# Performance work log

Measured on AMD Instinct MI355X. Metric: run time of the kernel, lower is better.

Reference implementation:

```python
import jax, jax.numpy as jnp
import numpy as np

ALPHA = 0.25
GAMMA = 2.0
DELTA = 0.5
BREAK_W = 1.0
REG_W = 1.0
CLASS_WEIGHT_TABLE = jnp.array([1.0, 4.0, 3.0, 2.0], dtype=jnp.float32)  # classes 0..3
LOG_CLAMP = -100.0  # torch BCELoss clamps log terms at -100

B, T = 2048, 16384


def setup_inputs() -> dict:
    key = jax.random.key(0)
    k1, k2, k3, k4 = jax.random.split(key, 4)
    break_predictions = jax.random.uniform(k1, (B, T), dtype=jnp.float32)
    regression_predictions = jax.random.uniform(k2, (B, T), dtype=jnp.float32) * 3.0
    break_targets = jax.random.uniform(k3, (B, T), dtype=jnp.float32)
    regression_targets = jax.random.uniform(k4, (B, T), dtype=jnp.float32) * 3.0
    return {
        "break_predictions": break_predictions,
        "regression_predictions": regression_predictions,
        "break_targets": break_targets,
        "regression_targets": regression_targets,
    }


def _bce(p, t):
    # torch BCELoss: mean of -(t*log(p) + (1-t)*log(1-p)), logs clamped at -100
    log_p = jnp.maximum(jnp.log(p), LOG_CLAMP)
    log_1p = jnp.maximum(jnp.log1p(-p), LOG_CLAMP)
    return jnp.mean(-(t * log_p + (1.0 - t) * log_1p))


def _duration_aware_focal(y_pred, y_true):
    y_pred = y_pred.reshape(-1)
    y_true = y_true.reshape(-1)
    # class-weight gather: round + clamp to [0,3], index a 4-entry table
    cls_idx = jnp.clip(jnp.round(y_true), 0.0, 3.0).astype(jnp.int32)
    weights = CLASS_WEIGHT_TABLE[cls_idx]
    d = jnp.abs(y_pred - y_true)
    focal = jnp.clip(d / DELTA, 0.0, 1.0) ** GAMMA
    # smooth L1 with beta=DELTA
    base = jnp.where(d < DELTA, 0.5 * d * d / DELTA, d - 0.5 * DELTA)
    return jnp.mean(ALPHA * focal * base * weights)


def reference(break_predictions, regression_predictions, break_targets, regression_targets):
    bt = jnp.clip(break_targets, 0.0, 1.0)
    bp = jnp.clip(break_predictions, 0.0, 1.0)
    break_loss = _bce(bp, bt)
    regression_loss = _duration_aware_focal(regression_predictions, regression_targets)
    total = BREAK_W * break_loss + REG_W * regression_loss
    return (total, break_loss, regression_loss)
```

## Files before the change

### kernel.cpp

```cpp
#include <hip/hip_runtime.h>


constexpr int BLOCK = 256;
constexpr int HGRID = 2048;
constexpr int GRID  = 2 * HGRID;

__device__ __forceinline__ void bce_elem(float pv, float tv, float& acc) {
    constexpr float CLAMP2 = -144.26950408889634f;
    float pc = fminf(fmaxf(pv, 0.0f), 1.0f);
    float tc = fminf(fmaxf(tv, 0.0f), 1.0f);
    float lp  = fmaxf(__log2f(pc),        CLAMP2);
    float l1p = fmaxf(__log2f(1.0f - pc), CLAMP2);
    acc -= l1p + tc * (lp - l1p);
}

__device__ __forceinline__ void focal_elem(float qv, float sv, float& acc) {
    float d = fabsf(qv - sv);
    float f = fminf(d + d, 1.0f);
    float base = (d < 0.5f) ? (d * d) : (d - 0.25f);
    float r = fminf(fmaxf(__builtin_rintf(sv), 0.0f), 3.0f);
    float w = (r == 0.0f) ? 1.0f : (r == 1.0f) ? 4.0f : (r == 2.0f) ? 3.0f : 2.0f;
    acc += (f * f) * base * w;
}

__global__ __launch_bounds__(BLOCK) void partial_kernel(
    const float4* __restrict__ bp4, const float4* __restrict__ rp4,
    const float4* __restrict__ bt4, const float4* __restrict__ rt4,
    float* __restrict__ partials, int n4, int n)
{
    const int stride = HGRID * BLOCK;
    float a0 = 0.0f, a1 = 0.0f;
    const bool isB = (blockIdx.x < HGRID);
    const int  vb  = isB ? blockIdx.x : blockIdx.x - HGRID;

    if (isB) {
        for (int i = vb * BLOCK + threadIdx.x; i < n4; i += stride) {
            float4 p = bp4[i];
            float4 t = bt4[i];
            bce_elem(p.x, t.x, a0);
            bce_elem(p.y, t.y, a1);
            bce_elem(p.z, t.z, a0);
            bce_elem(p.w, t.w, a1);
        }
        if (vb == 0) {
            const float* bp = (const float*)bp4;
            const float* bt = (const float*)bt4;
            for (int k = n4 * 4 + threadIdx.x; k < n; k += BLOCK)
                bce_elem(bp[k], bt[k], a0);
        }
    } else {
        for (int i = vb * BLOCK + threadIdx.x; i < n4; i += stride) {
            float4 q = rp4[i];
            float4 s = rt4[i];
            focal_elem(q.x, s.x, a0);
            focal_elem(q.y, s.y, a1);
            focal_elem(q.z, s.z, a0);
            focal_elem(q.w, s.w, a1);
        }
        if (vb == 0) {
            const float* rp = (const float*)rp4;
            const float* rt = (const float*)rt4;
            for (int k = n4 * 4 + threadIdx.x; k < n; k += BLOCK)
                focal_elem(rp[k], rt[k], a0);
        }
    }

    float acc = a0 + a1;
    #pragma unroll
    for (int off = 32; off > 0; off >>= 1)
        acc += __shfl_down(acc, off, 64);
    __shared__ float sA[BLOCK / 64];
    const int lane = threadIdx.x & 63;
    const int wid  = threadIdx.x >> 6;
    if (lane == 0) sA[wid] = acc;
    __syncthreads();
    if (threadIdx.x == 0) {
        float v = 0.0f;
        #pragma unroll
        for (int w = 0; w < BLOCK / 64; ++w) v += sA[w];
        partials[blockIdx.x] = v;
    }
}

__global__ __launch_bounds__(BLOCK) void final_kernel(
    const float* __restrict__ partials, float* __restrict__ out, double invN)
{
    double accB = 0.0, accR = 0.0;
    for (int i = threadIdx.x; i < HGRID; i += BLOCK) {
        accB += (double)partials[i];
        accR += (double)partials[HGRID + i];
    }
    #pragma unroll
    for (int off = 32; off > 0; off >>= 1) {
        accB += __shfl_down(accB, off, 64);
        accR += __shfl_down(accR, off, 64);
    }
    __shared__ double dB[BLOCK / 64], dR[BLOCK / 64];
    const int lane = threadIdx.x & 63;
    const int wid  = threadIdx.x >> 6;
    if (lane == 0) { dB[wid] = accB; dR[wid] = accR; }
    __syncthreads();
    if (threadIdx.x == 0) {
        double b = 0.0, r = 0.0;
        #pragma unroll
        for (int w = 0; w < BLOCK / 64; ++w) { b += dB[w]; r += dR[w]; }
        const double bm = b * 0.6931471805599453 * invN;
        const double rm = r * 0.25 * invN;
        out[0] = (float)(bm + rm);
        out[1] = (float)bm;
        out[2] = (float)rm;
    }
}

extern "C" void kernel_launch(void* const* d_in, const int* in_sizes, int n_in,
                              void* d_out, int out_size, void* d_ws, size_t ws_size,
                              hipStream_t stream) {
    const float* bp = (const float*)d_in[0];
    const float* rp = (const float*)d_in[1];
    const float* bt = (const float*)d_in[2];
    const float* rt = (const float*)d_in[3];
    const int n  = in_sizes[0];
    const int n4 = n / 4;
    float* partials = (float*)d_ws;

    partial_kernel<<<GRID, BLOCK, 0, stream>>>(
        (const float4*)bp, (const float4*)rp, (const float4*)bt, (const float4*)rt,
        partials, n4, n);
    final_kernel<<<1, BLOCK, 0, stream>>>(partials, (float*)d_out, 1.0 / (double)n);
}
```

Measured before the change: 102.4 us.

## Stage grid-stride loads through LDS with triple-buffered async global_load_lds

Replaces the direct float4 global loads in the streaming reduction with a three-slot LDS ring filled by global_load_lds, keeping two iterations of loads in flight per thread and waiting on vmcnt before consuming each slot. The goal is deeper memory-level parallelism for a bandwidth-bound reduction over 4×32M floats. It adds 24KB of shared memory per block, which can lower occupancy, and puts LDS reads plus manual waitcnt and scheduling barriers on the critical path. A fallback path handles sizes that do not divide evenly.

```diff
diff --git a/kernel.cpp b/kernel.cpp
--- a/kernel.cpp
+++ b/kernel.cpp
@@ -4,6 +4,21 @@
 constexpr int BLOCK = 256;
 constexpr int HGRID = 2048;
 constexpr int GRID  = 2 * HGRID;
+constexpr int BUFS  = 3;
+
+typedef float f32x4 __attribute__((ext_vector_type(4)));
+
+__device__ __forceinline__ void stage16(const float* g, void* l) {
+    __builtin_amdgcn_global_load_lds(
+        (const __attribute__((address_space(1))) void*)g,
+        (__attribute__((address_space(3))) void*)l,
+        16, 0, 0);
+}
+
+#define WAITV(N) do { \
+    asm volatile("s_waitcnt vmcnt(" #N ")" ::: "memory"); \
+    __builtin_amdgcn_sched_barrier(0); \
+} while (0)
 
 __device__ __forceinline__ void bce_elem(float pv, float tv, float& acc) {
     constexpr float CLAMP2 = -144.26950408889634f;
@@ -23,47 +38,82 @@
     acc += (f * f) * base * w;
 }
 
+template <bool IS_BCE>
+__device__ __forceinline__ void accum4(const f32x4& p, const f32x4& t,
+                                       float& a0, float& a1) {
+    if (IS_BCE) {
+        bce_elem(p[0], t[0], a0); bce_elem(p[1], t[1], a1);
+        bce_elem(p[2], t[2], a0); bce_elem(p[3], t[3], a1);
+    } else {
+        focal_elem(p[0], t[0], a0); focal_elem(p[1], t[1], a1);
+        focal_elem(p[2], t[2], a0); focal_elem(p[3], t[3], a1);
+    }
+}
+
+template <bool IS_BCE>
+__device__ __forceinline__ void run_half(
+    const f32x4* __restrict__ P, const f32x4* __restrict__ T,
+    f32x4* smem, int vb, int n4, int n, float& a0, float& a1)
+{
+    const int tid    = (int)threadIdx.x;
+    const int wid    = tid >> 6;
+    const int stride = HGRID * BLOCK;
+    const int base   = vb * BLOCK + tid;
+    const int iters  = n4 / stride;
+
+    if ((n4 % stride) == 0 && iters >= BUFS) {
+        #pragma unroll
+        for (int d = 0; d < 2; ++d) {
+            stage16((const float*)(P + base + (long)d * stride),
+                    (void*)(smem + (d * 2 + 0) * BLOCK + wid * 64));
+            stage16((const float*)(T + base + (long)d * stride),
+                    (void*)(smem + (d * 2 + 1) * BLOCK + wid * 64));
+        }
+        for (int it = 0; it < iters; ++it) {
+            const int slot = it % BUFS;
+            if (it < iters - 1) WAITV(2);
+            else                WAITV(0);
+            if (it + 2 < iters) {
+                const int s2 = (it + 2) % BUFS;
+                stage16((const float*)(P + base + (long)(it + 2) * stride),
+                        (void*)(smem + (s2 * 2 + 0) * BLOCK + wid * 64));
+                stage16((const float*)(T + base + (long)(it + 2) * stride),
+                        (void*)(smem + (s2 * 2 + 1) * BLOCK + wid * 64));
+            }
+            __builtin_amdgcn_sched_barrier(0);
+            f32x4 p = smem[(slot * 2 + 0) * BLOCK + tid];
+            f32x4 t = smem[(slot * 2 + 1) * BLOCK + tid];
+            accum4<IS_BCE>(p, t, a0, a1);
+        }
+    } else {
+        for (int i = base; i < n4; i += stride) {
+            f32x4 p = P[i];
+            f32x4 t = T[i];
+            accum4<IS_BCE>(p, t, a0, a1);
+        }
+        if (vb == 0) {
+            const float* Pf = (const float*)P;
+            const float* Tf = (const float*)T;
+            for (int k = n4 * 4 + tid; k < n; k += BLOCK) {
+                if (IS_BCE) bce_elem(Pf[k], Tf[k], a0);
+                else        focal_elem(Pf[k], Tf[k], a0);
+            }
+        }
+    }
+}
+
 __global__ __launch_bounds__(BLOCK) void partial_kernel(
-    const float4* __restrict__ bp4, const float4* __restrict__ rp4,
-    const float4* __restrict__ bt4, const float4* __restrict__ rt4,
+    const f32x4* __restrict__ bp4, const f32x4* __restrict__ rp4,
+    const f32x4* __restrict__ bt4, const f32x4* __restrict__ rt4,
     float* __restrict__ partials, int n4, int n)
 {
-    const int stride = HGRID * BLOCK;
+    __shared__ f32x4 smem[BUFS * 2 * BLOCK];
     float a0 = 0.0f, a1 = 0.0f;
-    const bool isB = (blockIdx.x < HGRID);
+    const bool isB = (blockIdx.x < (unsigned)HGRID);
     const int  vb  = isB ? blockIdx.x : blockIdx.x - HGRID;
 
-    if (isB) {
-        for (int i = vb * BLOCK + threadIdx.x; i < n4; i += stride) {
-            float4 p = bp4[i];
-            float4 t = bt4[i];
-            bce_elem(p.x, t.x, a0);
-            bce_elem(p.y, t.y, a1);
-            bce_elem(p.z, t.z, a0);
-            bce_elem(p.w, t.w, a1);
-        }
-        if (vb == 0) {
-            const float* bp = (const float*)bp4;
-            const float* bt = (const float*)bt4;
-            for (int k = n4 * 4 + threadIdx.x; k < n; k += BLOCK)
-                bce_elem(bp[k], bt[k], a0);
-        }
-    } else {
-        for (int i = vb * BLOCK + threadIdx.x; i < n4; i += stride) {
-            float4 q = rp4[i];
-            float4 s = rt4[i];
-            focal_elem(q.x, s.x, a0);
-            focal_elem(q.y, s.y, a1);
-            focal_elem(q.z, s.z, a0);
-            focal_elem(q.w, s.w, a1);
-        }
-        if (vb == 0) {
-            const float* rp = (const float*)rp4;
-            const float* rt = (const float*)rt4;
-            for (int k = n4 * 4 + threadIdx.x; k < n; k += BLOCK)
-                focal_elem(rp[k], rt[k], a0);
-        }
-    }
+    if (isB) run_half<true >(bp4, bt4, smem, vb, n4, n, a0, a1);
+    else     run_half<false>(rp4, rt4, smem, vb, n4, n, a0, a1);
 
     float acc = a0 + a1;
     #pragma unroll
@@ -124,7 +174,7 @@
     float* partials = (float*)d_ws;
 
     partial_kernel<<<GRID, BLOCK, 0, stream>>>(
-        (const float4*)bp, (const float4*)rp, (const float4*)bt, (const float4*)rt,
+        (const f32x4*)bp, (const f32x4*)rp, (const f32x4*)bt, (const f32x4*)rt,
         partials, n4, n);
     final_kernel<<<1, BLOCK, 0, stream>>>(partials, (float*)d_out, 1.0 / (double)n);
 }
```

Measured after the change: 100.9 us (median of 3 runs). About the same (-1.5%).
